# Kernel optimization log

Measured on AMD Instinct MI355X. Metric: run time of the kernel, lower is better.

## Reference

```python
import jax, jax.numpy as jnp
import numpy as np

B, G, K, C, NT = 128, 64, 32, 256, 8192


def setup_inputs() -> dict:
    key = jax.random.key(0)
    ks = jax.random.split(key, 8)
    s = lambda fan_in: 1.0 / np.sqrt(fan_in)
    return {
        "patch_features": jax.random.normal(ks[0], (B, G, C), jnp.float32),
        "neighborhood": jax.random.normal(ks[1], (B, G, K, 3), jnp.float32),
        "codebook": jax.random.normal(ks[2], (NT, C), jnp.float32),
        "w1": jax.random.normal(ks[3], (512, C), jnp.float32) * s(C),
        "b1": jnp.zeros((512,), jnp.float32),
        "w2": jax.random.normal(ks[4], (256, 512), jnp.float32) * s(512),
        "b2": jnp.zeros((256,), jnp.float32),
        "w3": jax.random.normal(ks[5], (3 * K, 256), jnp.float32) * s(256),
        "b3": jnp.zeros((3 * K,), jnp.float32),
    }


def reference(patch_features, neighborhood, codebook, w1, b1, w2, b2, w3, b3):
    b, g, c = patch_features.shape
    k = neighborhood.shape[2]
    # squared euclidean distances to codebook (argmin equals argmin of cdist p=2)
    d2 = (
        jnp.sum(patch_features * patch_features, -1, keepdims=True)
        - 2.0 * jnp.einsum("bgc,nc->bgn", patch_features, codebook)
        + jnp.sum(codebook * codebook, -1)
    )  # [B,G,NT]
    token_ids = jnp.argmin(d2, axis=-1)          # [B,G]
    quantized = codebook[token_ids]              # [B,G,C] gather
    # 1x1 Conv1d stack == per-token MLP
    h = jax.nn.relu(jnp.einsum("bgc,oc->bgo", quantized, w1) + b1)
    h = jax.nn.relu(jnp.einsum("bgc,oc->bgo", h, w2) + b2)
    rec = jnp.einsum("bgc,oc->bgo", h, w3) + b3  # [B,G,3K]
    rec = rec.reshape(b * g, k, 3)
    gt = neighborhood.reshape(b * g, k, 3)
    # Chamfer distance L2 (squared) both directions
    diff = rec[:, :, None, :] - gt[:, None, :, :]  # [BG,K,K,3]
    dd = jnp.sum(diff * diff, -1)                  # [BG,K,K]
    loss = jnp.mean(jnp.min(dd, axis=2)) + jnp.mean(jnp.min(dd, axis=1))
    return loss
```

## Files before the change

### kernel.cpp

```cpp
#include <hip/hip_runtime.h>
#include <hip/hip_bf16.h>
#include <float.h>

#define NTOK 8192
#define NCB  8192
#define CDIM 256
#define KPTS 32
#define SQNT 24.0f
#define INV_CFOLD (SQNT * SQNT * 64.0f)

typedef __attribute__((ext_vector_type(8))) short short8;
typedef __attribute__((ext_vector_type(4))) float f32x4;
typedef __attribute__((ext_vector_type(4))) int i32x4;
typedef unsigned int u32;
typedef unsigned long long u64;

__device__ __forceinline__ void gl_lds16(const void* g, void* l) {
  __builtin_amdgcn_global_load_lds(
      (const __attribute__((address_space(1))) u32*)(g),
      (__attribute__((address_space(3))) u32*)(l), 16, 0, 0);
}

__device__ __forceinline__ ushort bf16_rne(float x) {
  u32 u = __float_as_uint(x);
  return (ushort)((u + 0x7fffu + ((u >> 16) & 1u)) >> 16);
}

__device__ __forceinline__ int pack4i8(int a, int b, int c, int d) {
  return (a & 0xff) | ((b & 0xff) << 8) | ((c & 0xff) << 16) | ((d & 0xff) << 24);
}

__global__ __launch_bounds__(256) void prep_k(
    const float* __restrict__ pf, const float* __restrict__ cb,
    const float* __restrict__ w1, const float* __restrict__ w2,
    const float* __restrict__ w3,
    i32x4* __restrict__ pf1, i32x4* __restrict__ pf2,
    i32x4* __restrict__ cb1, i32x4* __restrict__ cb2,
    ushort* __restrict__ cb_bf, ushort* __restrict__ w1s,
    ushort* __restrict__ w2s, ushort* __restrict__ w3s,
    float* __restrict__ cnorm, float* __restrict__ out) {
  __shared__ float cred[4][16];
  if (blockIdx.x == 0 && threadIdx.x == 0) out[0] = 0.f;
  int gid = blockIdx.x * 4 + (threadIdx.x >> 6);
  int wv = threadIdx.x >> 6;
  int lane = threadIdx.x & 63, r16 = lane & 15, quad = lane >> 4;
  if (gid < 4096) {
    bool is_cb = gid >= 2048;
    int t = is_cb ? gid - 2048 : gid;
    int tile = t >> 2, kb = t & 3;
    const float* src = is_cb ? cb : pf;
    int row = tile * 16 + r16;
    const float* sp = src + (size_t)row * CDIM + kb * 64 + quad * 16;
    float4 v0 = ((const float4*)sp)[0];
    float4 v1 = ((const float4*)sp)[1];
    float4 v2 = ((const float4*)sp)[2];
    float4 v3 = ((const float4*)sp)[3];
    float x[16] = {v0.x, v0.y, v0.z, v0.w, v1.x, v1.y, v1.z, v1.w,
                   v2.x, v2.y, v2.z, v2.w, v3.x, v3.y, v3.z, v3.w};
    int q1[16], q2[16];
    float s = 0.f;
#pragma unroll
    for (int e = 0; e < 16; e++) {
      float as = x[e] * SQNT;
      float a1 = rintf(as);
      a1 = fminf(fmaxf(a1, -127.f), 127.f);
      float a2 = rintf((as - a1) * 128.f);
      a2 = fminf(fmaxf(a2, -127.f), 127.f);
      q1[e] = (int)a1;
      q2[e] = (int)a2;
      s += x[e] * x[e];
    }
    i32x4 p1 = {pack4i8(q1[0], q1[1], q1[2], q1[3]),
                pack4i8(q1[4], q1[5], q1[6], q1[7]),
                pack4i8(q1[8], q1[9], q1[10], q1[11]),
                pack4i8(q1[12], q1[13], q1[14], q1[15])};
    i32x4 p2 = {pack4i8(q2[0], q2[1], q2[2], q2[3]),
                pack4i8(q2[4], q2[5], q2[6], q2[7]),
                pack4i8(q2[8], q2[9], q2[10], q2[11]),
                pack4i8(q2[12], q2[13], q2[14], q2[15])};
    size_t o = (size_t)t * 64 + lane;
    (is_cb ? cb1 : pf1)[o] = p1;
    (is_cb ? cb2 : pf2)[o] = p2;
    if (is_cb) {
      int kb32 = 2 * kb + (quad >> 1);
      int slot0 = ((2 * quad) & 3) * 16 + r16;
      int slot1 = ((2 * quad + 1) & 3) * 16 + r16;
      size_t bo = ((size_t)tile * 8 + kb32) * 512;
      short8 vh0 = {(short)bf16_rne(x[0]), (short)bf16_rne(x[1]),
                    (short)bf16_rne(x[2]), (short)bf16_rne(x[3]),
                    (short)bf16_rne(x[4]), (short)bf16_rne(x[5]),
                    (short)bf16_rne(x[6]), (short)bf16_rne(x[7])};
      short8 vh1 = {(short)bf16_rne(x[8]), (short)bf16_rne(x[9]),
                    (short)bf16_rne(x[10]), (short)bf16_rne(x[11]),
                    (short)bf16_rne(x[12]), (short)bf16_rne(x[13]),
                    (short)bf16_rne(x[14]), (short)bf16_rne(x[15])};
      *(short8*)(cb_bf + bo + (size_t)slot0 * 8) = vh0;
      *(short8*)(cb_bf + bo + (size_t)slot1 * 8) = vh1;
      s += __shfl_xor(s, 16, 64);
      s += __shfl_xor(s, 32, 64);
      if (quad == 0) cred[wv][r16] = s;
      __syncthreads();
      if (threadIdx.x < 16) {
        int ctile = blockIdx.x - 512;
        cnorm[ctile * 16 + threadIdx.x] =
            cred[0][threadIdx.x] + cred[1][threadIdx.x] +
            cred[2][threadIdx.x] + cred[3][threadIdx.x];
      }
    }
  } else if (gid < 4656) {
    int t = gid - 4096;
    const float* src;
    ushort* dst;
    int KB;
    if (t < 256)      { src = w1; dst = w1s; KB = 8; }
    else if (t < 512) { src = w2; dst = w2s; KB = 16; t -= 256; }
    else              { src = w3; dst = w3s; KB = 8;  t -= 512; }
    int tile = t / KB, kb = t - tile * KB, K = KB * 32;
    int row = tile * 16 + r16;
    const float* sp = src + (size_t)row * K + kb * 32 + quad * 8;
    float4 a = ((const float4*)sp)[0];
    float4 b = ((const float4*)sp)[1];
    short8 vh = {(short)bf16_rne(a.x), (short)bf16_rne(a.y),
                 (short)bf16_rne(a.z), (short)bf16_rne(a.w),
                 (short)bf16_rne(b.x), (short)bf16_rne(b.y),
                 (short)bf16_rne(b.z), (short)bf16_rne(b.w)};
    *(short8*)(dst + ((size_t)tile * KB + kb) * 512 + lane * 8) = vh;
  }
}

__global__ __launch_bounds__(256, 2) void argmin_k(
    const char* __restrict__ A1g, const char* __restrict__ A2g,
    const char* __restrict__ B1g, const char* __restrict__ B2g,
    const float* __restrict__ cnorm, u64* __restrict__ pkeys) {
  extern __shared__ char lds[];
  char* A1 = lds;
  char* A2 = lds + 32768;
  char* Bb = lds + 65536;
  int tid = threadIdx.x;
  int ns = blockIdx.x, mt = blockIdx.y;
  int wv = tid >> 6, lane = tid & 63;
  int quad = lane >> 4, r16 = lane & 15;
  int wr = wv >> 1, wc = wv & 1;

  int bvi[4][4], bii[4][4];
#pragma unroll
  for (int i = 0; i < 4; i++)
#pragma unroll
    for (int r = 0; r < 4; r++) { bvi[i][r] = 0x7fffffff; bii[i][r] = 0x7fffffff; }

#pragma unroll
  for (int u = 0; u < 16; ++u) {
    int c = wv + u * 4;
    const char* src = (c < 32) ? A1g : A2g;
    char* dst = (c < 32) ? A1 : A2;
    int cc = c & 31;
    gl_lds16(src + ((size_t)(mt * 8 + (cc >> 2)) * 4 + (cc & 3)) * 1024 + lane * 16,
             dst + cc * 1024);
  }

  i32x4 am[4][4], ac[4][4];
  for (int s = 0; s < 16; ++s) {
    int nts = s >> 2, kb = s & 3;
    int nt = ns * 4 + nts;
#pragma unroll
    for (int u = 0; u < 4; ++u) {
      int c = wv * 4 + u;
      const char* src = (c < 8) ? B1g : B2g;
      int gt = nt * 8 + (c & 7);
      gl_lds16(src + ((size_t)gt * 4 + kb) * 1024 + lane * 16, Bb + c * 1024);
    }
    __syncthreads();
    if (kb == 0) {
#pragma unroll
      for (int i = 0; i < 4; i++)
#pragma unroll
        for (int j = 0; j < 4; j++) {
          am[i][j] = (i32x4){0, 0, 0, 0};
          ac[i][j] = (i32x4){0, 0, 0, 0};
        }
    }
    i32x4 f1[4], f2[4], g1[4], g2[4];
#pragma unroll
    for (int i = 0; i < 4; i++) {
      f1[i] = *(const i32x4*)(A1 + ((wr * 4 + i) * 4 + kb) * 1024 + lane * 16);
      f2[i] = *(const i32x4*)(A2 + ((wr * 4 + i) * 4 + kb) * 1024 + lane * 16);
    }
#pragma unroll
    for (int j = 0; j < 4; j++) {
      g1[j] = *(const i32x4*)(Bb + (wc * 4 + j) * 1024 + lane * 16);
      g2[j] = *(const i32x4*)(Bb + (8 + wc * 4 + j) * 1024 + lane * 16);
    }
#pragma unroll
    for (int i = 0; i < 4; i++)
#pragma unroll
      for (int j = 0; j < 4; j++) {
        am[i][j] = __builtin_amdgcn_mfma_i32_16x16x64_i8(f1[i], g1[j], am[i][j], 0, 0, 0);
        ac[i][j] = __builtin_amdgcn_mfma_i32_16x16x64_i8(f1[i], g2[j], ac[i][j], 0, 0, 0);
        ac[i][j] = __builtin_amdgcn_mfma_i32_16x16x64_i8(f2[i], g1[j], ac[i][j], 0, 0, 0);
      }
    if (kb == 3) {
#pragma unroll
      for (int j = 0; j < 4; j++) {
        int col = nt * 128 + wc * 64 + j * 16 + r16;
        int cni = __float2int_rn(cnorm[col] * INV_CFOLD);
#pragma unroll
        for (int i = 0; i < 4; i++)
#pragma unroll
          for (int r = 0; r < 4; r++) {
            int di = cni - (am[i][j][r] * 128 + ac[i][j][r]);
            if (di < bvi[i][r]) { bvi[i][r] = di; bii[i][r] = col; }
          }
      }
    }
    __syncthreads();
  }
#pragma unroll
  for (int m = 1; m < 16; m <<= 1) {
#pragma unroll
    for (int i = 0; i < 4; i++)
#pragma unroll
      for (int r = 0; r < 4; r++) {
        int ov = __shfl_xor(bvi[i][r], m, 64);
        int oi = __shfl_xor(bii[i][r], m, 64);
        if (ov < bvi[i][r] || (ov == bvi[i][r] && oi < bii[i][r])) {
          bvi[i][r] = ov;
          bii[i][r] = oi;
        }
      }
  }
  if (r16 == 0) {
#pragma unroll
    for (int i = 0; i < 4; i++)
#pragma unroll
      for (int r = 0; r < 4; r++) {
        int row = mt * 128 + wr * 64 + i * 16 + quad * 4 + r;
        u32 mk = (u32)(bvi[i][r] + (1 << 30));
        pkeys[(size_t)(ns * 2 + wc) * NTOK + row] = ((u64)mk << 32) | (u32)bii[i][r];
      }
  }
}

__global__ __launch_bounds__(512) void mlp_fused_k(
    const u64* __restrict__ pkeys, const ushort* __restrict__ cb_bf,
    const ushort* __restrict__ w1s, const float* __restrict__ b1,
    const ushort* __restrict__ w2s, const float* __restrict__ b2,
    const ushort* __restrict__ w3s, const float* __restrict__ b3,
    const float* __restrict__ neigh, float* __restrict__ out) {
  __shared__ ushort qs_h2[8 * 512];
  __shared__ ushort h1s[16 * 512];
  __shared__ float rec[16 * 96];
  __shared__ float gts[16 * 96];
  __shared__ int ids[16];
  __shared__ float wsum[8];

  int tid = threadIdx.x;
  int t0 = blockIdx.x * 16;
  int wv = tid >> 6, lane = tid & 63;
  int quad = lane >> 4, r16 = lane & 15;

  {
    int row_l = tid >> 5, sl = tid & 31;
    u64 best = pkeys[(size_t)sl * NTOK + t0 + row_l];
#pragma unroll
    for (int m = 1; m < 32; m <<= 1) {
      u64 o = __shfl_xor((unsigned long long)best, m, 64);
      if (o < best) best = o;
    }
    if (sl == 0) ids[row_l] = (int)(u32)best;
  }
  __syncthreads();

  {
    int kb = wv;
    int id = ids[r16];
    short8 v = *(const short8*)(cb_bf + ((size_t)(id >> 4) * 8 + kb) * 512 +
                                (size_t)((id & 15) + quad * 16) * 8);
    *(short8*)(qs_h2 + (size_t)kb * 512 + lane * 8) = v;
  }
  __syncthreads();

  short8 fa1[8];
#pragma unroll
  for (int kb = 0; kb < 8; kb++)
    fa1[kb] = *(const short8*)(qs_h2 + (size_t)kb * 512 + lane * 8);
  __syncthreads();

#pragma unroll
  for (int jj = 0; jj < 4; ++jj) {
    int jt = wv + jj * 8;
    f32x4 acc = (f32x4){0.f, 0.f, 0.f, 0.f};
#pragma unroll
    for (int kb = 0; kb < 8; kb++) {
      short8 fb = *(const short8*)(w1s + ((size_t)jt * 8 + kb) * 512 + lane * 8);
      acc = __builtin_amdgcn_mfma_f32_16x16x32_bf16(fa1[kb], fb, acc, 0, 0, 0);
    }
    int col = jt * 16 + r16;
    float bj = b1[col];
#pragma unroll
    for (int reg = 0; reg < 4; reg++) {
      int row_l = quad * 4 + reg;
      float v = fmaxf(acc[reg] + bj, 0.f);
      size_t o = (size_t)(col >> 5) * 512 +
                 (size_t)(((col >> 3) & 3) * 16 + row_l) * 8 + (col & 7);
      h1s[o] = bf16_rne(v);
    }
  }
  __syncthreads();

#pragma unroll
  for (int jj = 0; jj < 2; ++jj) {
    int jt = wv + jj * 8;
    f32x4 acc = (f32x4){0.f, 0.f, 0.f, 0.f};
#pragma unroll
    for (int kb = 0; kb < 16; kb++) {
      short8 fa = *(const short8*)(h1s + (size_t)kb * 512 + lane * 8);
      short8 fb = *(const short8*)(w2s + ((size_t)jt * 16 + kb) * 512 + lane * 8);
      acc = __builtin_amdgcn_mfma_f32_16x16x32_bf16(fa, fb, acc, 0, 0, 0);
    }
    int col = jt * 16 + r16;
    float bj = b2[col];
#pragma unroll
    for (int reg = 0; reg < 4; reg++) {
      int row_l = quad * 4 + reg;
      float v = fmaxf(acc[reg] + bj, 0.f);
      size_t o = (size_t)(col >> 5) * 512 +
                 (size_t)(((col >> 3) & 3) * 16 + row_l) * 8 + (col & 7);
      qs_h2[o] = bf16_rne(v);
    }
  }
  __syncthreads();

  if (tid < 384) {
    int t = tid / 24, c = (tid - t * 24) * 4;
    *(float4*)(gts + (size_t)t * 96 + c) =
        *(const float4*)(neigh + (size_t)(t0 + t) * 96 + c);
  }

  if (wv < 6) {
    int jt = wv;
    f32x4 acc = (f32x4){0.f, 0.f, 0.f, 0.f};
#pragma unroll
    for (int kb = 0; kb < 8; kb++) {
      short8 fa = *(const short8*)(qs_h2 + (size_t)kb * 512 + lane * 8);
      short8 fb = *(const short8*)(w3s + ((size_t)jt * 8 + kb) * 512 + lane * 8);
      acc = __builtin_amdgcn_mfma_f32_16x16x32_bf16(fa, fb, acc, 0, 0, 0);
    }
    int col = jt * 16 + r16;
    float bj = b3[col];
#pragma unroll
    for (int reg = 0; reg < 4; reg++) {
      int row_l = quad * 4 + reg;
      rec[(size_t)row_l * 96 + col] = acc[reg] + bj;
    }
  }
  __syncthreads();

  float local = 0.f;
  {
    int t = tid >> 5, i = tid & 31;
    float rx = rec[t * 96 + 3 * i], ry = rec[t * 96 + 3 * i + 1], rz = rec[t * 96 + 3 * i + 2];
    float gx = gts[t * 96 + 3 * i], gy = gts[t * 96 + 3 * i + 1], gz = gts[t * 96 + 3 * i + 2];
    float mA = FLT_MAX, mB = FLT_MAX;
#pragma unroll
    for (int j = 0; j < 32; j++) {
      float dx = rx - gts[t * 96 + 3 * j], dy = ry - gts[t * 96 + 3 * j + 1],
            dz = rz - gts[t * 96 + 3 * j + 2];
      float d = dx * dx + dy * dy + dz * dz;
      mA = fminf(mA, d);
      dx = rec[t * 96 + 3 * j] - gx; dy = rec[t * 96 + 3 * j + 1] - gy;
      dz = rec[t * 96 + 3 * j + 2] - gz;
      d = dx * dx + dy * dy + dz * dz;
      mB = fminf(mB, d);
    }
    local = mA + mB;
  }
#pragma unroll
  for (int off = 32; off; off >>= 1) local += __shfl_down(local, off, 64);
  if (lane == 0) wsum[wv] = local;
  __syncthreads();
  if (tid == 0) {
    float s = 0.f;
#pragma unroll
    for (int w = 0; w < 8; w++) s += wsum[w];
    atomicAdd(out, s * (1.0f / (float)(NTOK * KPTS)));
  }
}

extern "C" void kernel_launch(void* const* d_in, const int* in_sizes, int n_in,
                              void* d_out, int out_size, void* d_ws, size_t ws_size,
                              hipStream_t stream) {
  const float* pf    = (const float*)d_in[0];
  const float* neigh = (const float*)d_in[1];
  const float* cb    = (const float*)d_in[2];
  const float* w1    = (const float*)d_in[3];
  const float* b1    = (const float*)d_in[4];
  const float* w2    = (const float*)d_in[5];
  const float* b2    = (const float*)d_in[6];
  const float* w3    = (const float*)d_in[7];
  const float* b3    = (const float*)d_in[8];
  float* out = (float*)d_out;
  char* base = (char*)d_ws;

  u64*   pkeys = (u64*)base;
  float* cnorm = (float*)(base + 0x200000);
  char*  pf1   = base + 0x210000;
  char*  pf2   = base + 0x410000;
  char*  cb1   = base + 0x610000;
  char*  cb2   = base + 0x810000;
  ushort* cb_bf = (ushort*)(base + 0xA10000);
  ushort* w1s   = (ushort*)(base + 0xE10000);
  ushort* w2s   = (ushort*)(base + 0xE50000);
  ushort* w3s   = (ushort*)(base + 0xE90000);

  prep_k<<<1164, 256, 0, stream>>>(pf, cb, w1, w2, w3,
                                   (i32x4*)pf1, (i32x4*)pf2, (i32x4*)cb1,
                                   (i32x4*)cb2, cb_bf, w1s, w2s, w3s, cnorm, out);
  argmin_k<<<dim3(16, 64), 256, 81920, stream>>>(pf1, pf2, cb1, cb2, cnorm, pkeys);
  mlp_fused_k<<<512, 512, 0, stream>>>(pkeys, cb_bf, w1s, b1, w2s, b2,
                                       w3s, b3, neigh, out);
}
```

Before: 160.4 us.

## Restructure int8 argmin GEMM with 32x32 MFMA, register-resident A and double-buffered B

Changes the quantized distance GEMM from 16x16x64 to 32x32x32 int8 MFMA, and re-lays out the packed feature and codebook arrays to match. The A operand (patch features) now lives in registers for the whole kernel instead of in LDS. Codebook tiles are double-buffered in LDS so the next half-K stage loads while the current one computes. The grid is reshaped to 4 column groups by 128 row tiles, which cuts the partial-key slots from 32 to 8 and simplifies the reduction in the MLP kernel. The aim is fewer LDS reads and barriers and more load/compute overlap, at the cost of register pressure and fewer blocks per row tile.

```diff
diff --git a/kernel.cpp b/kernel.cpp
--- a/kernel.cpp
+++ b/kernel.cpp
@@ -9,9 +9,13 @@
 #define SQNT 24.0f
 #define INV_CFOLD (SQNT * SQNT * 64.0f)
 
+#define CG   4
+#define NTPB 16
+
 typedef __attribute__((ext_vector_type(8))) short short8;
 typedef __attribute__((ext_vector_type(4))) float f32x4;
 typedef __attribute__((ext_vector_type(4))) int i32x4;
+typedef __attribute__((ext_vector_type(16))) int i32x16;
 typedef unsigned int u32;
 typedef unsigned long long u64;
 
@@ -78,7 +82,11 @@
                 pack4i8(q2[4], q2[5], q2[6], q2[7]),
                 pack4i8(q2[8], q2[9], q2[10], q2[11]),
                 pack4i8(q2[12], q2[13], q2[14], q2[15])};
-    size_t o = (size_t)t * 64 + lane;
+    int rt32 = tile >> 1;
+    int row_in = ((tile & 1) << 4) | r16;
+    int kc32 = (kb << 1) | (quad >> 1);
+    int k_half = quad & 1;
+    size_t o = (size_t)(rt32 * 8 + kc32) * 64 + k_half * 32 + row_in;
     (is_cb ? cb1 : pf1)[o] = p1;
     (is_cb ? cb2 : pf2)[o] = p2;
     if (is_cb) {
@@ -128,115 +136,120 @@
   }
 }
 
+__device__ __forceinline__ void stage_b(const char* __restrict__ B1g,
+                                        const char* __restrict__ B2g,
+                                        size_t ctb, int kh, char* dst,
+                                        int wv, int lane) {
+#pragma unroll
+  for (int u = 0; u < 8; ++u) {
+    int c = wv * 8 + u;
+    int lv = c >> 4, ct = (c >> 2) & 3, kc = (c & 3) + kh * 4;
+    const char* src = (lv ? B2g : B1g) +
+                      ((ctb + ct) * 8 + kc) * 1024 + (size_t)lane * 16;
+    gl_lds16(src, dst + c * 1024);
+  }
+}
+
+template <int KH>
+__device__ __forceinline__ void phase_mfma(const char* bcur, int wc, int lane,
+                                           const i32x4* a1, const i32x4* a2,
+                                           i32x16* am, i32x16* ac) {
+#pragma unroll
+  for (int kk = 0; kk < 4; ++kk) {
+#pragma unroll
+    for (int j = 0; j < 2; ++j) {
+      int ct = wc * 2 + j;
+      i32x4 b1 = *(const i32x4*)(bcur + (ct * 4 + kk) * 1024 + lane * 16);
+      i32x4 b2 = *(const i32x4*)(bcur + (16 + ct * 4 + kk) * 1024 + lane * 16);
+      am[j] = __builtin_amdgcn_mfma_i32_32x32x32_i8(a1[KH * 4 + kk], b1, am[j], 0, 0, 0);
+      ac[j] = __builtin_amdgcn_mfma_i32_32x32x32_i8(a1[KH * 4 + kk], b2, ac[j], 0, 0, 0);
+      ac[j] = __builtin_amdgcn_mfma_i32_32x32x32_i8(a2[KH * 4 + kk], b1, ac[j], 0, 0, 0);
+    }
+  }
+}
+
 __global__ __launch_bounds__(256, 2) void argmin_k(
     const char* __restrict__ A1g, const char* __restrict__ A2g,
     const char* __restrict__ B1g, const char* __restrict__ B2g,
     const float* __restrict__ cnorm, u64* __restrict__ pkeys) {
   extern __shared__ char lds[];
-  char* A1 = lds;
-  char* A2 = lds + 32768;
-  char* Bb = lds + 65536;
+  char* buf0 = lds;
+  char* buf1 = lds + 32768;
   int tid = threadIdx.x;
-  int ns = blockIdx.x, mt = blockIdx.y;
+  int cg = blockIdx.x, mt = blockIdx.y;
   int wv = tid >> 6, lane = tid & 63;
-  int quad = lane >> 4, r16 = lane & 15;
-  int wr = wv >> 1, wc = wv & 1;
-
-  int bvi[4][4], bii[4][4];
-#pragma unroll
-  for (int i = 0; i < 4; i++)
-#pragma unroll
-    for (int r = 0; r < 4; r++) { bvi[i][r] = 0x7fffffff; bii[i][r] = 0x7fffffff; }
-
-#pragma unroll
-  for (int u = 0; u < 16; ++u) {
-    int c = wv + u * 4;
-    const char* src = (c < 32) ? A1g : A2g;
-    char* dst = (c < 32) ? A1 : A2;
-    int cc = c & 31;
-    gl_lds16(src + ((size_t)(mt * 8 + (cc >> 2)) * 4 + (cc & 3)) * 1024 + lane * 16,
-             dst + cc * 1024);
-  }
-
-  i32x4 am[4][4], ac[4][4];
-  for (int s = 0; s < 16; ++s) {
-    int nts = s >> 2, kb = s & 3;
-    int nt = ns * 4 + nts;
-#pragma unroll
-    for (int u = 0; u < 4; ++u) {
-      int c = wv * 4 + u;
-      const char* src = (c < 8) ? B1g : B2g;
-      int gt = nt * 8 + (c & 7);
-      gl_lds16(src + ((size_t)gt * 4 + kb) * 1024 + lane * 16, Bb + c * 1024);
-    }
+  int rt = wv >> 1, wc = wv & 1;
+  int l31 = lane & 31, lh = lane >> 5;
+
+  i32x4 a1[8], a2[8];
+  {
+    int rtg = mt * 2 + rt;
+    const char* a1p = A1g + (size_t)rtg * 8192 + (size_t)lane * 16;
+    const char* a2p = A2g + (size_t)rtg * 8192 + (size_t)lane * 16;
+#pragma unroll
+    for (int kc = 0; kc < 8; ++kc) {
+      a1[kc] = *(const i32x4*)(a1p + kc * 1024);
+      a2[kc] = *(const i32x4*)(a2p + kc * 1024);
+    }
+  }
+
+  stage_b(B1g, B2g, (size_t)(cg * NTPB) * 4, 0, buf0, wv, lane);
+  __syncthreads();
+
+  int bvi[16], bii[16];
+#pragma unroll
+  for (int r = 0; r < 16; ++r) { bvi[r] = 0x7fffffff; bii[r] = 0x7fffffff; }
+
+  i32x16 am[2], ac[2];
+
+  for (int n = 0; n < NTPB; ++n) {
+    size_t ctb = (size_t)(cg * NTPB + n) * 4;
+    stage_b(B1g, B2g, ctb, 1, buf1, wv, lane);
+#pragma unroll
+    for (int j = 0; j < 2; ++j)
+#pragma unroll
+      for (int r = 0; r < 16; ++r) { am[j][r] = 0; ac[j][r] = 0; }
+    phase_mfma<0>(buf0, wc, lane, a1, a2, am, ac);
     __syncthreads();
-    if (kb == 0) {
-#pragma unroll
-      for (int i = 0; i < 4; i++)
-#pragma unroll
-        for (int j = 0; j < 4; j++) {
-          am[i][j] = (i32x4){0, 0, 0, 0};
-          ac[i][j] = (i32x4){0, 0, 0, 0};
-        }
-    }
-    i32x4 f1[4], f2[4], g1[4], g2[4];
-#pragma unroll
-    for (int i = 0; i < 4; i++) {
-      f1[i] = *(const i32x4*)(A1 + ((wr * 4 + i) * 4 + kb) * 1024 + lane * 16);
-      f2[i] = *(const i32x4*)(A2 + ((wr * 4 + i) * 4 + kb) * 1024 + lane * 16);
-    }
-#pragma unroll
-    for (int j = 0; j < 4; j++) {
-      g1[j] = *(const i32x4*)(Bb + (wc * 4 + j) * 1024 + lane * 16);
-      g2[j] = *(const i32x4*)(Bb + (8 + wc * 4 + j) * 1024 + lane * 16);
-    }
-#pragma unroll
-    for (int i = 0; i < 4; i++)
-#pragma unroll
-      for (int j = 0; j < 4; j++) {
-        am[i][j] = __builtin_amdgcn_mfma_i32_16x16x64_i8(f1[i], g1[j], am[i][j], 0, 0, 0);
-        ac[i][j] = __builtin_amdgcn_mfma_i32_16x16x64_i8(f1[i], g2[j], ac[i][j], 0, 0, 0);
-        ac[i][j] = __builtin_amdgcn_mfma_i32_16x16x64_i8(f2[i], g1[j], ac[i][j], 0, 0, 0);
-      }
-    if (kb == 3) {
-#pragma unroll
-      for (int j = 0; j < 4; j++) {
-        int col = nt * 128 + wc * 64 + j * 16 + r16;
+    if (n + 1 < NTPB) stage_b(B1g, B2g, ctb + 4, 0, buf0, wv, lane);
+    phase_mfma<1>(buf1, wc, lane, a1, a2, am, ac);
+    {
+      int colbase = (cg * NTPB + n) * 128 + wc * 64;
+#pragma unroll
+      for (int j = 0; j < 2; ++j) {
+        int col = colbase + j * 32 + l31;
         int cni = __float2int_rn(cnorm[col] * INV_CFOLD);
 #pragma unroll
-        for (int i = 0; i < 4; i++)
-#pragma unroll
-          for (int r = 0; r < 4; r++) {
-            int di = cni - (am[i][j][r] * 128 + ac[i][j][r]);
-            if (di < bvi[i][r]) { bvi[i][r] = di; bii[i][r] = col; }
-          }
-      }
-    }
-    __syncthreads();
-  }
-#pragma unroll
-  for (int m = 1; m < 16; m <<= 1) {
-#pragma unroll
-    for (int i = 0; i < 4; i++)
-#pragma unroll
-      for (int r = 0; r < 4; r++) {
-        int ov = __shfl_xor(bvi[i][r], m, 64);
-        int oi = __shfl_xor(bii[i][r], m, 64);
-        if (ov < bvi[i][r] || (ov == bvi[i][r] && oi < bii[i][r])) {
-          bvi[i][r] = ov;
-          bii[i][r] = oi;
+        for (int r = 0; r < 16; ++r) {
+          int di = cni - (am[j][r] * 128 + ac[j][r]);
+          if (di < bvi[r]) { bvi[r] = di; bii[r] = col; }
         }
       }
-  }
-  if (r16 == 0) {
-#pragma unroll
-    for (int i = 0; i < 4; i++)
-#pragma unroll
-      for (int r = 0; r < 4; r++) {
-        int row = mt * 128 + wr * 64 + i * 16 + quad * 4 + r;
-        u32 mk = (u32)(bvi[i][r] + (1 << 30));
-        pkeys[(size_t)(ns * 2 + wc) * NTOK + row] = ((u64)mk << 32) | (u32)bii[i][r];
+    }
+    __syncthreads();
+  }
+
+#pragma unroll
+  for (int m = 1; m < 32; m <<= 1) {
+#pragma unroll
+    for (int r = 0; r < 16; ++r) {
+      int ov = __shfl_xor(bvi[r], m, 64);
+      int oi = __shfl_xor(bii[r], m, 64);
+      if (ov < bvi[r] || (ov == bvi[r] && oi < bii[r])) {
+        bvi[r] = ov;
+        bii[r] = oi;
       }
+    }
+  }
+  if (l31 == 0) {
+    int rowb = mt * 64 + rt * 32 + 4 * lh;
+    size_t sbase = (size_t)(cg * 2 + wc) * NTOK;
+#pragma unroll
+    for (int r = 0; r < 16; ++r) {
+      int row = rowb + (r & 3) + 8 * (r >> 2);
+      u32 mk = (u32)(bvi[r] + (1 << 30));
+      pkeys[sbase + row] = ((u64)mk << 32) | (u32)bii[r];
+    }
   }
 }
 
@@ -258,11 +271,11 @@
   int wv = tid >> 6, lane = tid & 63;
   int quad = lane >> 4, r16 = lane & 15;
 
-  {
-    int row_l = tid >> 5, sl = tid & 31;
+  if (tid < 128) {
+    int row_l = tid >> 3, sl = tid & 7;
     u64 best = pkeys[(size_t)sl * NTOK + t0 + row_l];
 #pragma unroll
-    for (int m = 1; m < 32; m <<= 1) {
+    for (int m = 1; m < 8; m <<= 1) {
       u64 o = __shfl_xor((unsigned long long)best, m, 64);
       if (o < best) best = o;
     }
@@ -415,7 +428,7 @@
   prep_k<<<1164, 256, 0, stream>>>(pf, cb, w1, w2, w3,
                                    (i32x4*)pf1, (i32x4*)pf2, (i32x4*)cb1,
                                    (i32x4*)cb2, cb_bf, w1s, w2s, w3s, cnorm, out);
-  argmin_k<<<dim3(16, 64), 256, 81920, stream>>>(pf1, pf2, cb1, cb2, cnorm, pkeys);
+  argmin_k<<<dim3(CG, 128), 256, 65536, stream>>>(pf1, pf2, cb1, cb2, cnorm, pkeys);
   mlp_fused_k<<<512, 512, 0, stream>>>(pkeys, cb_bf, w1s, b1, w2s, b2,
                                        w3s, b3, neigh, out);
 }
```

After: 161.5 us. No clear change (+0.7%).
